# Optimization experiments

Hardware: AMD Instinct MI355X
Metric: run time of the kernel (lower is better)

## Reference

```python
import jax, jax.numpy as jnp
jax.config.update("jax_enable_x64", True)  # morton codes need int64 bit tricks
import numpy as np

B = 8
N_POINTS = 131072
PATCH = 32
STRIDE = 16
RES = 1024
D_MODEL = 256
L = (N_POINTS - PATCH) // STRIDE + 1  # 8191


def setup_inputs() -> dict:
    key = jax.random.key(0)
    ks = jax.random.split(key, 11)
    def lin_w(k, fin, fout):
        return (jax.random.normal(k, (fin, fout), jnp.float32) / np.sqrt(fin)).astype(jnp.float32)
    return {
        "points": jax.random.normal(ks[0], (B, N_POINTS, 3), jnp.float32),
        # LocalGeometryEncoder mlp: 3 -> 64 -> 128 (ReLU after both)
        "W1": lin_w(ks[1], 3, 64), "b1": jnp.zeros((64,), jnp.float32),
        "W2": lin_w(ks[2], 64, 128), "b2": jnp.zeros((128,), jnp.float32),
        # PositionalEncoding mlp: 3 -> 64 -> 128 (ReLU only after first)
        "Wp1": lin_w(ks[3], 3, 64), "bp1": jnp.zeros((64,), jnp.float32),
        "Wp2": lin_w(ks[4], 64, 128), "bp2": jnp.zeros((128,), jnp.float32),
        # projection: 256 -> d_model
        "Wproj": lin_w(ks[5], 256, D_MODEL), "bproj": jnp.zeros((D_MODEL,), jnp.float32),
    }


def _expand_bits(v):
    v = v.astype(jnp.int64)
    v = (v | (v << 32)) & jnp.int64(8725724278095871)
    v = (v | (v << 16)) & jnp.int64(8725728556220671)
    v = (v | (v << 8)) & jnp.int64(1157144660301377551)
    v = (v | (v << 4)) & jnp.int64(1207822528635744451)
    v = (v | (v << 2)) & jnp.int64(1317624576693539401)
    return v


def _morton_code(points):
    p_min = points.min(axis=1, keepdims=True)
    p_max = points.max(axis=1, keepdims=True)
    scale = jnp.clip(p_max - p_min, 1e-8, None)
    normed = (points - p_min) / scale
    q = jnp.clip((normed * (RES - 1)).astype(jnp.int64), 0, RES - 1)  # [B,N,3]
    return _expand_bits(q[..., 0]) * 4 + _expand_bits(q[..., 1]) * 2 + _expand_bits(q[..., 2])


def reference(points, W1, b1, W2, b2, Wp1, bp1, Wp2, bp2, Wproj, bproj):
    # z-order sort
    morton = _morton_code(points)                 # [B,N] int64
    sort_idx = jnp.argsort(morton, axis=1)        # [B,N]
    sp = jnp.take_along_axis(points, sort_idx[..., None], axis=1)  # [B,N,3]
    # sliding-window unfold -> [B,L,P,3]
    win = jnp.arange(L)[:, None] * STRIDE + jnp.arange(PATCH)[None, :]  # [L,P]
    patches = sp[:, win, :]
    # local geometry encoder
    centroids = patches.mean(axis=2)              # [B,L,3]
    local = patches - centroids[:, :, None, :]    # [B,L,P,3]
    h = jax.nn.relu(jnp.einsum('blpc,cd->blpd', local, W1) + b1)
    feat = jax.nn.relu(jnp.einsum('blpd,de->blpe', h, W2) + b2)  # [B,L,P,128]
    geo = feat.max(axis=2)                        # [B,L,128]
    # positional encoding of centroids
    pos = jax.nn.relu(centroids @ Wp1 + bp1) @ Wp2 + bp2  # [B,L,128]
    combined = jnp.concatenate([geo, pos], axis=-1)       # [B,L,256]
    tokens = combined @ Wproj + bproj                     # [B,L,d_model]
    return tokens, centroids, sort_idx
```

## Files before the change

kernel.cpp:

```cpp
#include <hip/hip_runtime.h>
#include <hip/hip_bf16.h>
#include <stdint.h>

#define B_SZ   8
#define N_PTS  131072
#define L_TOK  8191
#define M_TOK  (B_SZ * L_TOK)

typedef unsigned long long u64;
typedef unsigned int u32;
typedef unsigned short u16;
typedef __hip_bfloat16 bf16;
typedef float f32x4 __attribute__((ext_vector_type(4)));
typedef short bf16x8 __attribute__((ext_vector_type(8)));
typedef u32 u32x4 __attribute__((ext_vector_type(4)));

__device__ __forceinline__ u16 f2bf(float f) {
  u32 u = __float_as_uint(f);
  u32 r = u + 0x7FFFu + ((u >> 16) & 1u);
  return (u16)(r >> 16);
}
__device__ __forceinline__ float bf2f(u16 s) {
  return __uint_as_float(((u32)s) << 16);
}

__device__ __forceinline__ void split_pair(float h0, float h1, u32& hp, u32& lp) {
  asm("v_cvt_pk_bf16_f32 %0, %1, %2" : "=v"(hp) : "v"(h0), "v"(h1));
  float r0 = __uint_as_float(hp << 16);
  float r1 = __uint_as_float(hp & 0xFFFF0000u);
  asm("v_cvt_pk_bf16_f32 %0, %1, %2" : "=v"(lp) : "v"(h0 - r0), "v"(h1 - r1));
}
__device__ __forceinline__ bf16x8 asbf(u32x4 x) {
  union { u32x4 a; bf16x8 b; } u; u.a = x; return u.b;
}

__device__ __forceinline__ u32 f2u_mono(float f) {
  u32 u = __float_as_uint(f);
  return (u & 0x80000000u) ? ~u : (u | 0x80000000u);
}
__device__ __forceinline__ float u2f_mono(u32 u) {
  u32 b = (u & 0x80000000u) ? (u ^ 0x80000000u) : ~u;
  return __uint_as_float(b);
}

__global__ void init_mm_kernel(u32* mm) {
  int t = threadIdx.x;
  if (t < 48) mm[t] = ((t % 6) < 3) ? 0xFFFFFFFFu : 0u;
}

__global__ __launch_bounds__(256) void minmax_kernel(const float* __restrict__ pts,
                                                     u32* __restrict__ mm) {
  int b = blockIdx.x >> 6;
  int chunk = blockIdx.x & 63;
  int base = b * N_PTS + chunk * 2048;
  float mn0 = 3.4e38f, mn1 = 3.4e38f, mn2 = 3.4e38f;
  float mx0 = -3.4e38f, mx1 = -3.4e38f, mx2 = -3.4e38f;
  for (int i = threadIdx.x; i < 2048; i += 256) {
    const float* p = pts + (size_t)(base + i) * 3;
    float x = p[0], y = p[1], z = p[2];
    mn0 = fminf(mn0, x); mx0 = fmaxf(mx0, x);
    mn1 = fminf(mn1, y); mx1 = fmaxf(mx1, y);
    mn2 = fminf(mn2, z); mx2 = fmaxf(mx2, z);
  }
  __shared__ u32 smn[3], smx[3];
  if (threadIdx.x < 3) { smn[threadIdx.x] = 0xFFFFFFFFu; smx[threadIdx.x] = 0u; }
  __syncthreads();
  atomicMin(&smn[0], f2u_mono(mn0)); atomicMin(&smn[1], f2u_mono(mn1)); atomicMin(&smn[2], f2u_mono(mn2));
  atomicMax(&smx[0], f2u_mono(mx0)); atomicMax(&smx[1], f2u_mono(mx1)); atomicMax(&smx[2], f2u_mono(mx2));
  __syncthreads();
  if (threadIdx.x < 3)       atomicMin(&mm[b * 6 + threadIdx.x], smn[threadIdx.x]);
  else if (threadIdx.x < 6)  atomicMax(&mm[b * 6 + threadIdx.x], smx[threadIdx.x - 3]);
}

__device__ __forceinline__ u64 expand_bits(u64 v) {
  v = (v | (v << 32)) & 0x001F00000000FFFFull;
  v = (v | (v << 16)) & 0x001F0000FF0000FFull;
  v = (v | (v << 8))  & 0x100F00F00F00F00Full;
  v = (v | (v << 4))  & 0x10C30C30C30C30C3ull;
  v = (v | (v << 2))  & 0x1249249249249249ull;
  return v;
}

__device__ __forceinline__ long long quant1(float p, float mn, float mx) {
  float scale = fmaxf(mx - mn, 1e-8f);
  float num = p - mn;
  float rcp = 1.0f / scale;
  asm volatile("" : "+v"(rcp));
  float normed = num * rcp;
  asm volatile("" : "+v"(normed));
  float scaled = normed * 1023.0f;
  asm volatile("" : "+v"(scaled));
  long long q = (long long)scaled;
  q = q < 0 ? 0 : q; q = q > 1023 ? 1023 : q;
  return q;
}

__global__ __launch_bounds__(256) void morton_kernel(const float* __restrict__ pts,
                                                     const u32* __restrict__ mm,
                                                     u64* __restrict__ keys) {
  int gid = blockIdx.x * 256 + threadIdx.x;
  int b = gid >> 17;
  int i = gid & (N_PTS - 1);
  const u32* mb = mm + b * 6;
  float mn0 = u2f_mono(mb[0]), mn1 = u2f_mono(mb[1]), mn2 = u2f_mono(mb[2]);
  float mx0 = u2f_mono(mb[3]), mx1 = u2f_mono(mb[4]), mx2 = u2f_mono(mb[5]);
  const float* p = pts + (size_t)gid * 3;
  long long q0 = quant1(p[0], mn0, mx0);
  long long q1 = quant1(p[1], mn1, mx1);
  long long q2 = quant1(p[2], mn2, mx2);
  u64 m = expand_bits((u64)q0) * 4ull + expand_bits((u64)q1) * 2ull + expand_bits((u64)q2);
  keys[gid] = (m << 17) | (u64)i;
}

__global__ __launch_bounds__(512) void radix_hist(const u64* __restrict__ keys,
                                                  u32* __restrict__ hist, int shift) {
  int blk = blockIdx.x;
  int b = blk >> 6, c = blk & 63;
  int t = threadIdx.x;
  __shared__ u32 h[256];
  if (t < 256) h[t] = 0;
  __syncthreads();
  size_t base = ((size_t)b << 17) + (size_t)c * 2048;
  #pragma unroll
  for (int i = 0; i < 4; ++i) {
    u32 d = (u32)((keys[base + i * 512 + t] >> shift) & 255u);
    atomicAdd(&h[d], 1u);
  }
  __syncthreads();
  if (t < 256) hist[(blk << 8) + t] = h[t];
}

__global__ __launch_bounds__(256) void radix_scan_a(u32* __restrict__ hist,
                                                    u32* __restrict__ tot) {
  int blk = blockIdx.x;
  int b = blk >> 3, dg = blk & 7;
  int t = threadIdx.x;
  __shared__ u32 H[32 * 65];
  __shared__ u32 part[32 * 8];
  for (int i = t; i < 2048; i += 256) {
    int c = i >> 5, d5 = i & 31;
    H[d5 * 65 + c] = hist[((b * 64 + c) << 8) + dg * 32 + d5];
  }
  __syncthreads();
  int d5 = t & 31, sub = t >> 5;
  u32 s = 0;
  for (int c = sub * 8; c < sub * 8 + 8; ++c) s += H[d5 * 65 + c];
  part[d5 * 8 + sub] = s;
  __syncthreads();
  u32 run = 0;
  for (int k = 0; k < sub; ++k) run += part[d5 * 8 + k];
  if (sub == 7) tot[(b << 8) + dg * 32 + d5] = run + s;
  for (int c = sub * 8; c < sub * 8 + 8; ++c) {
    u32 x = H[d5 * 65 + c];
    H[d5 * 65 + c] = run;
    run += x;
  }
  __syncthreads();
  for (int i = t; i < 2048; i += 256) {
    int c = i >> 5, d5b = i & 31;
    hist[((b * 64 + c) << 8) + dg * 32 + d5b] = H[d5b * 65 + c];
  }
}

__global__ __launch_bounds__(256) void radix_scan_b(const u32* __restrict__ tot,
                                                    u32* __restrict__ dbase) {
  int b = blockIdx.x;
  int t = threadIdx.x;
  __shared__ u32 s[256];
  u32 my = tot[(b << 8) + t];
  s[t] = my;
  __syncthreads();
  for (int off = 1; off < 256; off <<= 1) {
    u32 v = (t >= off) ? s[t - off] : 0u;
    __syncthreads();
    s[t] += v;
    __syncthreads();
  }
  dbase[(b << 8) + t] = s[t] - my;
}

__global__ __launch_bounds__(512) void radix_scatter(const u64* __restrict__ keys_in,
                                                     u64* __restrict__ keys_out,
                                                     const u32* __restrict__ hist,
                                                     const u32* __restrict__ dbase,
                                                     int shift) {
  int blk = blockIdx.x;
  int b = blk >> 6, c = blk & 63;
  int t = threadIdx.x;
  int w = t >> 6, lane = t & 63;
  __shared__ u32 whist[8][256];
  __shared__ u32 gbase[256];
  for (int i = t; i < 2048; i += 512) ((u32*)whist)[i] = 0u;
  if (t < 256) gbase[t] = hist[(blk << 8) + t] + dbase[(b << 8) + t];
  __syncthreads();
  size_t base = ((size_t)b << 17) + (size_t)c * 2048;
  u64 key[4]; u32 dig[4]; u32 loff[4];
  #pragma unroll
  for (int i = 0; i < 4; ++i) {
    key[i] = keys_in[base + w * 256 + i * 64 + lane];
    dig[i] = (u32)((key[i] >> shift) & 255u);
  }
  #pragma unroll
  for (int i = 0; i < 4; ++i) {
    u64 m = ~0ull;
    #pragma unroll
    for (int k = 0; k < 8; ++k) {
      u64 bb = __ballot((dig[i] >> k) & 1u);
      m &= ((dig[i] >> k) & 1u) ? bb : ~bb;
    }
    u32 rank = (u32)__popcll(m & ((1ull << lane) - 1ull));
    u32 cnt = (u32)__popcll(m);
    int leader = (int)__ffsll((unsigned long long)m) - 1;
    u32 prev = 0;
    if (lane == leader) prev = atomicAdd(&whist[w][dig[i]], cnt);
    prev = __shfl(prev, leader);
    loff[i] = prev + rank;
  }
  __syncthreads();
  if (t < 256) {
    u32 run = 0;
    #pragma unroll
    for (int ww = 0; ww < 8; ++ww) { u32 v = whist[ww][t]; whist[ww][t] = run; run += v; }
  }
  __syncthreads();
  #pragma unroll
  for (int i = 0; i < 4; ++i) {
    u32 dst = gbase[dig[i]] + whist[w][dig[i]] + loff[i];
    keys_out[((size_t)b << 17) + dst] = key[i];
  }
}

__global__ __launch_bounds__(256) void extract_frag_kernel(
    const u64* __restrict__ keys, const float* __restrict__ pts,
    float* __restrict__ sp, float* __restrict__ sidx,
    const float* __restrict__ Wproj, const float* __restrict__ W2,
    const float* __restrict__ Wp2,
    u16* __restrict__ wfrag, u16* __restrict__ w2f, u16* __restrict__ wp2f) {
  int bid = blockIdx.x;
  int t = threadIdx.x;
  if (bid < 4096) {
    int gid = bid * 256 + t;
    u64 key = keys[gid];
    int idx = (int)(key & 0x1FFFFull);
    sidx[gid] = (float)idx;
    int b = gid >> 17;
    const float* src = pts + ((size_t)(b << 17) + idx) * 3;
    float* dst = sp + (size_t)gid * 3;
    dst[0] = src[0]; dst[1] = src[1]; dst[2] = src[2];
  } else {
    int fb = bid - 4096;
    if (fb < 256) {
      int e = fb * 256 + t;
      int k = e >> 8, n = e & 255;
      float v = Wproj[e];
      u16 hb = f2bf(v);
      u16 lb = f2bf(v - bf2f(hb));
      int ks = k >> 5, q = (k >> 3) & 3, j = k & 7;
      int nt = n >> 4, ln2 = n & 15;
      int base = ((ks * 16 + nt) * 64 + q * 16 + ln2) * 8 + j;
      wfrag[base] = hb;
      wfrag[65536 + base] = lb;
    } else {
      const float* W = (fb < 288) ? W2 : Wp2;
      u16* frag = (fb < 288) ? w2f : wp2f;
      int e = ((fb < 288) ? (fb - 256) : (fb - 288)) * 256 + t;
      int k = e >> 7, n = e & 127;
      float v = W[e];
      u16 hb = f2bf(v);
      u16 lb = f2bf(v - bf2f(hb));
      int kc = k >> 5, q = (k >> 3) & 3, j = k & 7;
      int nt = n >> 4, ln2 = n & 15;
      int base = ((kc * 8 + nt) * 64 + q * 16 + ln2) * 8 + j;
      frag[base] = hb;
      frag[8192 + base] = lb;
    }
  }
}

__global__ __launch_bounds__(512) void patch_kernel(
    const float* __restrict__ sp,
    const float* __restrict__ W1, const float* __restrict__ b1,
    const u16* __restrict__ W2g, const float* __restrict__ b2,
    const float* __restrict__ Wp1, const float* __restrict__ bp1,
    const u16* __restrict__ Wp2g, const float* __restrict__ bp2,
    bf16* __restrict__ comb, float* __restrict__ cent_out) {
  __shared__ float ptsS[6192];
  __shared__ float cenS[384];
  __shared__ float w1p[256];
  __shared__ float wpp[256];
  __shared__ float b2s[128];
  __shared__ float bp2s[128];
  __shared__ __align__(16) u16 W2frag[16384];

  int t = threadIdx.x;
  int bib = blockIdx.x;
  int b = blockIdx.y;
  int l0 = bib * 128;
  int pcount = min(128, L_TOK - l0);

  {
    const float4* src4 = (const float4*)(sp + (size_t)b * (N_PTS * 3) + (size_t)l0 * 48);
    int nvec = min(1548, ((N_PTS - l0 * 16) * 3) >> 2);
    float4* dst4 = (float4*)ptsS;
    for (int i = t; i < nvec; i += 512) dst4[i] = src4[i];
  }
  {
    const float4* s4 = (const float4*)W2g;
    float4* d4 = (float4*)W2frag;
    for (int i = t; i < 2048; i += 512) d4[i] = s4[i];
  }
  if (t < 64) {
    w1p[t] = W1[t]; w1p[64 + t] = W1[64 + t];
    w1p[128 + t] = W1[128 + t]; w1p[192 + t] = b1[t];
  } else if (t < 128) {
    int i = t - 64;
    wpp[i] = Wp1[i]; wpp[64 + i] = Wp1[64 + i];
    wpp[128 + i] = Wp1[128 + i]; wpp[192 + i] = bp1[i];
  } else if (t < 256) {
    b2s[t - 128] = b2[t - 128];
  } else if (t < 384) {
    bp2s[t - 256] = bp2[t - 256];
  }
  __syncthreads();

  if (t < 384) {
    int pa = t / 3, c = t - pa * 3;
    if (pa < pcount) {
      float s = 0.f;
      for (int i = 0; i < 32; ++i) {
        int ii = (i + pa) & 31;
        s += ptsS[(pa * 16 + ii) * 3 + c];
      }
      float cv = s * (1.0f / 32.0f);
      cenS[pa * 3 + c] = cv;
      cent_out[(size_t)(b * L_TOK + l0 + pa) * 3 + c] = cv;
    }
  }
  __syncthreads();

  int w = t >> 6, lane = t & 63, ln = lane & 15, quad = lane >> 4;
  const bf16x8* Bf = (const bf16x8*)W2frag;

  for (int ig = 0; ig < 16; ++ig) {
    int ll = w * 16 + ig;
    if (ll >= pcount) break;
    float cx = cenS[ll * 3], cy = cenS[ll * 3 + 1], cz = cenS[ll * 3 + 2];
    float xs[2], ys[2], zs[2];
    #pragma unroll
    for (int mt = 0; mt < 2; ++mt) {
      int row = ll * 16 + mt * 16 + ln;
      xs[mt] = ptsS[row * 3] - cx;
      ys[mt] = ptsS[row * 3 + 1] - cy;
      zs[mt] = ptsS[row * 3 + 2] - cz;
    }
    u32x4 Ahi[2][2], Alo[2][2];
    #pragma unroll
    for (int kc = 0; kc < 2; ++kc)
      #pragma unroll
      for (int w4 = 0; w4 < 4; ++w4) {
        int col = kc * 32 + quad * 8 + w4 * 2;
        float wx0 = w1p[col],     wy0 = w1p[64 + col],     wz0 = w1p[128 + col],     wb0 = w1p[192 + col];
        float wx1 = w1p[col + 1], wy1 = w1p[64 + col + 1], wz1 = w1p[128 + col + 1], wb1 = w1p[192 + col + 1];
        #pragma unroll
        for (int mt = 0; mt < 2; ++mt) {
          float h0 = fmaxf(fmaf(xs[mt], wx0, fmaf(ys[mt], wy0, fmaf(zs[mt], wz0, wb0))), 0.f);
          float h1 = fmaxf(fmaf(xs[mt], wx1, fmaf(ys[mt], wy1, fmaf(zs[mt], wz1, wb1))), 0.f);
          u32 hp, lp;
          split_pair(h0, h1, hp, lp);
          Ahi[mt][kc][w4] = hp;
          Alo[mt][kc][w4] = lp;
        }
      }
    bf16x8 Ah[2][2], Al[2][2];
    #pragma unroll
    for (int mt = 0; mt < 2; ++mt)
      #pragma unroll
      for (int kc = 0; kc < 2; ++kc) { Ah[mt][kc] = asbf(Ahi[mt][kc]); Al[mt][kc] = asbf(Alo[mt][kc]); }

    size_t tokoff = (size_t)(b * L_TOK + l0 + ll) * 256;
    #pragma unroll
    for (int half = 0; half < 2; ++half) {
      f32x4 acc[2][4];
      #pragma unroll
      for (int mt = 0; mt < 2; ++mt)
        #pragma unroll
        for (int n4 = 0; n4 < 4; ++n4) acc[mt][n4] = (f32x4){0.f, 0.f, 0.f, 0.f};
      #pragma unroll
      for (int n4 = 0; n4 < 4; ++n4) {
        int nt = half * 4 + n4;
        bf16x8 Bh0 = Bf[(0 * 8 + nt) * 64 + lane];
        bf16x8 Bh1 = Bf[(1 * 8 + nt) * 64 + lane];
        bf16x8 Bl0 = Bf[1024 + (0 * 8 + nt) * 64 + lane];
        bf16x8 Bl1 = Bf[1024 + (1 * 8 + nt) * 64 + lane];
        #pragma unroll
        for (int mt = 0; mt < 2; ++mt) {
          acc[mt][n4] = __builtin_amdgcn_mfma_f32_16x16x32_bf16(Ah[mt][0], Bh0, acc[mt][n4], 0, 0, 0);
          acc[mt][n4] = __builtin_amdgcn_mfma_f32_16x16x32_bf16(Ah[mt][1], Bh1, acc[mt][n4], 0, 0, 0);
          acc[mt][n4] = __builtin_amdgcn_mfma_f32_16x16x32_bf16(Al[mt][0], Bh0, acc[mt][n4], 0, 0, 0);
          acc[mt][n4] = __builtin_amdgcn_mfma_f32_16x16x32_bf16(Al[mt][1], Bh1, acc[mt][n4], 0, 0, 0);
          acc[mt][n4] = __builtin_amdgcn_mfma_f32_16x16x32_bf16(Ah[mt][0], Bl0, acc[mt][n4], 0, 0, 0);
          acc[mt][n4] = __builtin_amdgcn_mfma_f32_16x16x32_bf16(Ah[mt][1], Bl1, acc[mt][n4], 0, 0, 0);
        }
      }
      #pragma unroll
      for (int n4 = 0; n4 < 4; ++n4) {
        int col = (half * 4 + n4) * 16 + ln;
        float bv = b2s[col];
        float m = 0.f;
        #pragma unroll
        for (int mt = 0; mt < 2; ++mt)
          #pragma unroll
          for (int r = 0; r < 4; ++r) m = fmaxf(m, acc[mt][n4][r] + bv);
        m = fmaxf(m, __shfl_xor(m, 16));
        m = fmaxf(m, __shfl_xor(m, 32));
        if (lane < 16) comb[tokoff + col] = __float2bfloat16(m);
      }
    }
  }

  {
    int lrow = w * 16 + ln;
    int lcl = min(lrow, pcount - 1);
    float cx = cenS[lcl * 3], cy = cenS[lcl * 3 + 1], cz = cenS[lcl * 3 + 2];
    u32x4 Ahi[2], Alo[2];
    #pragma unroll
    for (int kc = 0; kc < 2; ++kc)
      #pragma unroll
      for (int w4 = 0; w4 < 4; ++w4) {
        int col = kc * 32 + quad * 8 + w4 * 2;
        float h0 = fmaxf(fmaf(cx, wpp[col], fmaf(cy, wpp[64 + col], fmaf(cz, wpp[128 + col], wpp[192 + col]))), 0.f);
        float h1 = fmaxf(fmaf(cx, wpp[col + 1], fmaf(cy, wpp[64 + col + 1], fmaf(cz, wpp[128 + col + 1], wpp[192 + col + 1]))), 0.f);
        u32 hp, lp;
        split_pair(h0, h1, hp, lp);
        Ahi[kc][w4] = hp;
        Alo[kc][w4] = lp;
      }
    bf16x8 A0h = asbf(Ahi[0]), A1h = asbf(Ahi[1]), A0l = asbf(Alo[0]), A1l = asbf(Alo[1]);
    const bf16x8* Pf = (const bf16x8*)Wp2g;
    f32x4 acc[8];
    #pragma unroll
    for (int nt = 0; nt < 8; ++nt) acc[nt] = (f32x4){0.f, 0.f, 0.f, 0.f};
    #pragma unroll
    for (int nt = 0; nt < 8; ++nt) {
      bf16x8 Bh0 = Pf[(0 * 8 + nt) * 64 + lane];
      bf16x8 Bh1 = Pf[(8 + nt) * 64 + lane];
      bf16x8 Bl0 = Pf[1024 + (0 * 8 + nt) * 64 + lane];
      bf16x8 Bl1 = Pf[1024 + (8 + nt) * 64 + lane];
      acc[nt] = __builtin_amdgcn_mfma_f32_16x16x32_bf16(A0h, Bh0, acc[nt], 0, 0, 0);
      acc[nt] = __builtin_amdgcn_mfma_f32_16x16x32_bf16(A1h, Bh1, acc[nt], 0, 0, 0);
      acc[nt] = __builtin_amdgcn_mfma_f32_16x16x32_bf16(A0l, Bh0, acc[nt], 0, 0, 0);
      acc[nt] = __builtin_amdgcn_mfma_f32_16x16x32_bf16(A1l, Bh1, acc[nt], 0, 0, 0);
      acc[nt] = __builtin_amdgcn_mfma_f32_16x16x32_bf16(A0h, Bl0, acc[nt], 0, 0, 0);
      acc[nt] = __builtin_amdgcn_mfma_f32_16x16x32_bf16(A1h, Bl1, acc[nt], 0, 0, 0);
    }
    #pragma unroll
    for (int nt = 0; nt < 8; ++nt)
      #pragma unroll
      for (int r = 0; r < 4; ++r) {
        int lr = w * 16 + quad * 4 + r;
        if (lr < pcount) {
          float v = acc[nt][r] + bp2s[nt * 16 + ln];
          comb[(size_t)(b * L_TOK + l0 + lr) * 256 + 128 + nt * 16 + ln] = __float2bfloat16(v);
        }
      }
  }
}

__global__ __launch_bounds__(256) void proj_mfma(const bf16* __restrict__ A,
                                                 const u16* __restrict__ fragG,
                                                 const float* __restrict__ bias,
                                                 float* __restrict__ C) {
  int t = threadIdx.x;
  int w = t >> 6, lane = t & 63, ln = lane & 15, quad = lane >> 4;
  int mg = blockIdx.x >> 1;
  int nh = blockIdx.x & 1;
  int tile0 = mg * 16 + w * 4;
  const bf16x8* Bf = (const bf16x8*)fragG;

  bf16x8 Af[4][8];
  const bf16x8 zero8 = (bf16x8){0, 0, 0, 0, 0, 0, 0, 0};
  #pragma unroll
  for (int mt = 0; mt < 4; ++mt) {
    int row = (tile0 + mt) * 16 + ln;
    bool ok = row < M_TOK;
    const bf16x8* ap = (const bf16x8*)(A + (size_t)(ok ? row : 0) * 256);
    #pragma unroll
    for (int ks = 0; ks < 8; ++ks) {
      bf16x8 v = ap[ks * 4 + quad];
      Af[mt][ks] = ok ? v : zero8;
    }
  }

  for (int nt2 = 0; nt2 < 8; ++nt2) {
    int nt = nh * 8 + nt2;
    f32x4 acc[4];
    #pragma unroll
    for (int mt = 0; mt < 4; ++mt) acc[mt] = (f32x4){0.f, 0.f, 0.f, 0.f};
    #pragma unroll
    for (int ks = 0; ks < 8; ++ks) {
      bf16x8 Bh = Bf[(ks * 16 + nt) * 64 + lane];
      bf16x8 Bl = Bf[8192 + (ks * 16 + nt) * 64 + lane];
      #pragma unroll
      for (int mt = 0; mt < 4; ++mt)
        acc[mt] = __builtin_amdgcn_mfma_f32_16x16x32_bf16(Af[mt][ks], Bh, acc[mt], 0, 0, 0);
      #pragma unroll
      for (int mt = 0; mt < 4; ++mt)
        acc[mt] = __builtin_amdgcn_mfma_f32_16x16x32_bf16(Af[mt][ks], Bl, acc[mt], 0, 0, 0);
    }
    int col = nt * 16 + ln;
    float bv = bias[col];
    #pragma unroll
    for (int mt = 0; mt < 4; ++mt)
      #pragma unroll
      for (int r = 0; r < 4; ++r) {
        int row = (tile0 + mt) * 16 + quad * 4 + r;
        if (row < M_TOK) C[(size_t)row * 256 + col] = acc[mt][r] + bv;
      }
  }
}

extern "C" void kernel_launch(void* const* d_in, const int* in_sizes, int n_in,
                              void* d_out, int out_size, void* d_ws, size_t ws_size,
                              hipStream_t stream) {
  const float* points = (const float*)d_in[0];
  const float* W1 = (const float*)d_in[1];
  const float* b1 = (const float*)d_in[2];
  const float* W2 = (const float*)d_in[3];
  const float* b2 = (const float*)d_in[4];
  const float* Wp1 = (const float*)d_in[5];
  const float* bp1 = (const float*)d_in[6];
  const float* Wp2 = (const float*)d_in[7];
  const float* bp2 = (const float*)d_in[8];
  const float* Wproj = (const float*)d_in[9];
  const float* bproj = (const float*)d_in[10];

  float* out = (float*)d_out;
  float* tokens = out;
  float* cents  = out + 16775168;
  float* sidx   = out + 16971752;

  char* ws = (char*)d_ws;
  u32* mm     = (u32*)ws;
  u64* keysA  = (u64*)(ws + 256);
  float* sp   = (float*)(ws + 256 + 8388608);
  char* combB = ws + 256 + 8388608 + 12582912;
  bf16* comb  = (bf16*)combB;
  u64* keysB  = (u64*)combB;
  u32* hist   = (u32*)(combB + 8388608);
  u32* totG   = (u32*)(combB + 8388608 + 2097152);
  u32* dbase  = (u32*)(combB + 8388608 + 2097152 + 8192);
  u16* wfrag  = (u16*)(ws + 256);
  u16* w2fg   = (u16*)(ws + 256 + 262144);
  u16* wp2fg  = (u16*)(ws + 256 + 262144 + 32768);

  init_mm_kernel<<<1, 64, 0, stream>>>(mm);
  minmax_kernel<<<512, 256, 0, stream>>>(points, mm);
  morton_kernel<<<4096, 256, 0, stream>>>(points, mm, keysA);

  const int shifts[4] = {17, 25, 33, 41};
  u64* src = keysA; u64* dst = keysB;
  for (int p = 0; p < 4; ++p) {
    radix_hist<<<512, 512, 0, stream>>>(src, hist, shifts[p]);
    radix_scan_a<<<64, 256, 0, stream>>>(hist, totG);
    radix_scan_b<<<8, 256, 0, stream>>>(totG, dbase);
    radix_scatter<<<512, 512, 0, stream>>>(src, dst, hist, dbase, shifts[p]);
    u64* tmp = src; src = dst; dst = tmp;
  }

  extract_frag_kernel<<<4416, 256, 0, stream>>>(src, points, sp, sidx,
                                                Wproj, W2, Wp2, wfrag, w2fg, wp2fg);
  patch_kernel<<<dim3(64, 8), 512, 0, stream>>>(sp, W1, b1, w2fg, b2,
                                                Wp1, bp1, wp2fg, bp2, comb, cents);
  proj_mfma<<<512, 256, 0, stream>>>(comb, wfrag, bproj, tokens);
}
```

Before: 352.1 us.

## Fuse radix digit-total scan into scatter and final pass into gather

Digit totals are now accumulated with global atomics in the histogram kernel, and each scatter block redoes the small 256-entry exclusive scan itself, so the separate scan_b kernel goes away. The last radix pass writes the sorted indices and gathered points directly instead of writing keys and running a separate extract kernel. The init kernel becomes memsets. This cuts kernel launches and one full pass over the keys, at the cost of redundant per-block scans and extra global atomics.

```diff
diff --git a/kernel.cpp b/kernel.cpp
--- a/kernel.cpp
+++ b/kernel.cpp
@@ -41,11 +41,6 @@
 __device__ __forceinline__ float u2f_mono(u32 u) {
   u32 b = (u & 0x80000000u) ? (u ^ 0x80000000u) : ~u;
   return __uint_as_float(b);
-}
-
-__global__ void init_mm_kernel(u32* mm) {
-  int t = threadIdx.x;
-  if (t < 48) mm[t] = ((t % 6) < 3) ? 0xFFFFFFFFu : 0u;
 }
 
 __global__ __launch_bounds__(256) void minmax_kernel(const float* __restrict__ pts,
@@ -68,8 +63,8 @@
   atomicMin(&smn[0], f2u_mono(mn0)); atomicMin(&smn[1], f2u_mono(mn1)); atomicMin(&smn[2], f2u_mono(mn2));
   atomicMax(&smx[0], f2u_mono(mx0)); atomicMax(&smx[1], f2u_mono(mx1)); atomicMax(&smx[2], f2u_mono(mx2));
   __syncthreads();
-  if (threadIdx.x < 3)       atomicMin(&mm[b * 6 + threadIdx.x], smn[threadIdx.x]);
-  else if (threadIdx.x < 6)  atomicMax(&mm[b * 6 + threadIdx.x], smx[threadIdx.x - 3]);
+  if (threadIdx.x < 3)       atomicMin(&mm[b * 3 + threadIdx.x], smn[threadIdx.x]);
+  else if (threadIdx.x < 6)  atomicMax(&mm[24 + b * 3 + threadIdx.x - 3], smx[threadIdx.x - 3]);
 }
 
 __device__ __forceinline__ u64 expand_bits(u64 v) {
@@ -101,9 +96,8 @@
   int gid = blockIdx.x * 256 + threadIdx.x;
   int b = gid >> 17;
   int i = gid & (N_PTS - 1);
-  const u32* mb = mm + b * 6;
-  float mn0 = u2f_mono(mb[0]), mn1 = u2f_mono(mb[1]), mn2 = u2f_mono(mb[2]);
-  float mx0 = u2f_mono(mb[3]), mx1 = u2f_mono(mb[4]), mx2 = u2f_mono(mb[5]);
+  float mn0 = u2f_mono(mm[b * 3]), mn1 = u2f_mono(mm[b * 3 + 1]), mn2 = u2f_mono(mm[b * 3 + 2]);
+  float mx0 = u2f_mono(mm[24 + b * 3]), mx1 = u2f_mono(mm[24 + b * 3 + 1]), mx2 = u2f_mono(mm[24 + b * 3 + 2]);
   const float* p = pts + (size_t)gid * 3;
   long long q0 = quant1(p[0], mn0, mx0);
   long long q1 = quant1(p[1], mn1, mx1);
@@ -113,7 +107,8 @@
 }
 
 __global__ __launch_bounds__(512) void radix_hist(const u64* __restrict__ keys,
-                                                  u32* __restrict__ hist, int shift) {
+                                                  u32* __restrict__ hist,
+                                                  u32* __restrict__ tot, int shift) {
   int blk = blockIdx.x;
   int b = blk >> 6, c = blk & 63;
   int t = threadIdx.x;
@@ -127,11 +122,14 @@
     atomicAdd(&h[d], 1u);
   }
   __syncthreads();
-  if (t < 256) hist[(blk << 8) + t] = h[t];
-}
-
-__global__ __launch_bounds__(256) void radix_scan_a(u32* __restrict__ hist,
-                                                    u32* __restrict__ tot) {
+  if (t < 256) {
+    u32 v = h[t];
+    hist[(blk << 8) + t] = v;
+    if (v) atomicAdd(&tot[(b << 8) + t], v);
+  }
+}
+
+__global__ __launch_bounds__(256) void radix_scan_a(u32* __restrict__ hist) {
   int blk = blockIdx.x;
   int b = blk >> 3, dg = blk & 7;
   int t = threadIdx.x;
@@ -149,7 +147,6 @@
   __syncthreads();
   u32 run = 0;
   for (int k = 0; k < sub; ++k) run += part[d5 * 8 + k];
-  if (sub == 7) tot[(b << 8) + dg * 32 + d5] = run + s;
   for (int c = sub * 8; c < sub * 8 + 8; ++c) {
     u32 x = H[d5 * 65 + c];
     H[d5 * 65 + c] = run;
@@ -162,27 +159,10 @@
   }
 }
 
-__global__ __launch_bounds__(256) void radix_scan_b(const u32* __restrict__ tot,
-                                                    u32* __restrict__ dbase) {
-  int b = blockIdx.x;
-  int t = threadIdx.x;
-  __shared__ u32 s[256];
-  u32 my = tot[(b << 8) + t];
-  s[t] = my;
-  __syncthreads();
-  for (int off = 1; off < 256; off <<= 1) {
-    u32 v = (t >= off) ? s[t - off] : 0u;
-    __syncthreads();
-    s[t] += v;
-    __syncthreads();
-  }
-  dbase[(b << 8) + t] = s[t] - my;
-}
-
 __global__ __launch_bounds__(512) void radix_scatter(const u64* __restrict__ keys_in,
                                                      u64* __restrict__ keys_out,
                                                      const u32* __restrict__ hist,
-                                                     const u32* __restrict__ dbase,
+                                                     const u32* __restrict__ tot,
                                                      int shift) {
   int blk = blockIdx.x;
   int b = blk >> 6, c = blk & 63;
@@ -190,9 +170,23 @@
   int w = t >> 6, lane = t & 63;
   __shared__ u32 whist[8][256];
   __shared__ u32 gbase[256];
+  __shared__ u32 sd[256];
   for (int i = t; i < 2048; i += 512) ((u32*)whist)[i] = 0u;
-  if (t < 256) gbase[t] = hist[(blk << 8) + t] + dbase[(b << 8) + t];
-  __syncthreads();
+  u32 my = 0;
+  if (t < 256) {
+    my = tot[(b << 8) + t];
+    sd[t] = my;
+    gbase[t] = hist[(blk << 8) + t];
+  }
+  __syncthreads();
+  #pragma unroll
+  for (int off = 1; off < 256; off <<= 1) {
+    u32 v = (t >= off && t < 256) ? sd[t - off] : 0u;
+    __syncthreads();
+    if (t < 256) sd[t] += v;
+    __syncthreads();
+  }
+  if (t < 256) gbase[t] += sd[t] - my;
   size_t base = ((size_t)b << 17) + (size_t)c * 2048;
   u64 key[4]; u32 dig[4]; u32 loff[4];
   #pragma unroll
@@ -230,27 +224,19 @@
   }
 }
 
-__global__ __launch_bounds__(256) void extract_frag_kernel(
-    const u64* __restrict__ keys, const float* __restrict__ pts,
-    float* __restrict__ sp, float* __restrict__ sidx,
+__global__ __launch_bounds__(512) void scatter_final(
+    const u64* __restrict__ keys_in, const u32* __restrict__ hist,
+    const u32* __restrict__ tot,
+    const float* __restrict__ pts, float* __restrict__ sp, float* __restrict__ sidx,
     const float* __restrict__ Wproj, const float* __restrict__ W2,
     const float* __restrict__ Wp2,
     u16* __restrict__ wfrag, u16* __restrict__ w2f, u16* __restrict__ wp2f) {
   int bid = blockIdx.x;
   int t = threadIdx.x;
-  if (bid < 4096) {
-    int gid = bid * 256 + t;
-    u64 key = keys[gid];
-    int idx = (int)(key & 0x1FFFFull);
-    sidx[gid] = (float)idx;
-    int b = gid >> 17;
-    const float* src = pts + ((size_t)(b << 17) + idx) * 3;
-    float* dst = sp + (size_t)gid * 3;
-    dst[0] = src[0]; dst[1] = src[1]; dst[2] = src[2];
-  } else {
-    int fb = bid - 4096;
-    if (fb < 256) {
-      int e = fb * 256 + t;
+  if (bid >= 512) {
+    int fb = bid - 512;
+    if (fb < 128) {
+      int e = fb * 512 + t;
       int k = e >> 8, n = e & 255;
       float v = Wproj[e];
       u16 hb = f2bf(v);
@@ -261,9 +247,9 @@
       wfrag[base] = hb;
       wfrag[65536 + base] = lb;
     } else {
-      const float* W = (fb < 288) ? W2 : Wp2;
-      u16* frag = (fb < 288) ? w2f : wp2f;
-      int e = ((fb < 288) ? (fb - 256) : (fb - 288)) * 256 + t;
+      const float* W = (fb < 144) ? W2 : Wp2;
+      u16* frag = (fb < 144) ? w2f : wp2f;
+      int e = ((fb < 144) ? (fb - 128) : (fb - 144)) * 512 + t;
       int k = e >> 7, n = e & 127;
       float v = W[e];
       u16 hb = f2bf(v);
@@ -274,6 +260,69 @@
       frag[base] = hb;
       frag[8192 + base] = lb;
     }
+    return;
+  }
+  int blk = bid;
+  int b = blk >> 6, c = blk & 63;
+  int w = t >> 6, lane = t & 63;
+  __shared__ u32 whist[8][256];
+  __shared__ u32 gbase[256];
+  __shared__ u32 sd[256];
+  for (int i = t; i < 2048; i += 512) ((u32*)whist)[i] = 0u;
+  u32 my = 0;
+  if (t < 256) {
+    my = tot[(b << 8) + t];
+    sd[t] = my;
+    gbase[t] = hist[(blk << 8) + t];
+  }
+  __syncthreads();
+  #pragma unroll
+  for (int off = 1; off < 256; off <<= 1) {
+    u32 v = (t >= off && t < 256) ? sd[t - off] : 0u;
+    __syncthreads();
+    if (t < 256) sd[t] += v;
+    __syncthreads();
+  }
+  if (t < 256) gbase[t] += sd[t] - my;
+  size_t base = ((size_t)b << 17) + (size_t)c * 2048;
+  u64 key[4]; u32 dig[4]; u32 loff[4];
+  #pragma unroll
+  for (int i = 0; i < 4; ++i) {
+    key[i] = keys_in[base + w * 256 + i * 64 + lane];
+    dig[i] = (u32)((key[i] >> 41) & 255u);
+  }
+  #pragma unroll
+  for (int i = 0; i < 4; ++i) {
+    u64 m = ~0ull;
+    #pragma unroll
+    for (int k = 0; k < 8; ++k) {
+      u64 bb = __ballot((dig[i] >> k) & 1u);
+      m &= ((dig[i] >> k) & 1u) ? bb : ~bb;
+    }
+    u32 rank = (u32)__popcll(m & ((1ull << lane) - 1ull));
+    u32 cnt = (u32)__popcll(m);
+    int leader = (int)__ffsll((unsigned long long)m) - 1;
+    u32 prev = 0;
+    if (lane == leader) prev = atomicAdd(&whist[w][dig[i]], cnt);
+    prev = __shfl(prev, leader);
+    loff[i] = prev + rank;
+  }
+  __syncthreads();
+  if (t < 256) {
+    u32 run = 0;
+    #pragma unroll
+    for (int ww = 0; ww < 8; ++ww) { u32 v = whist[ww][t]; whist[ww][t] = run; run += v; }
+  }
+  __syncthreads();
+  #pragma unroll
+  for (int i = 0; i < 4; ++i) {
+    u32 dst = gbase[dig[i]] + whist[w][dig[i]] + loff[i];
+    int idx = (int)(key[i] & 0x1FFFFull);
+    u32 gid = ((u32)b << 17) + dst;
+    sidx[gid] = (float)idx;
+    const float* s = pts + ((size_t)(b << 17) + idx) * 3;
+    float* dp = sp + (size_t)gid * 3;
+    dp[0] = s[0]; dp[1] = s[1]; dp[2] = s[2];
   }
 }
 
@@ -548,27 +597,29 @@
   u64* keysB  = (u64*)combB;
   u32* hist   = (u32*)(combB + 8388608);
   u32* totG   = (u32*)(combB + 8388608 + 2097152);
-  u32* dbase  = (u32*)(combB + 8388608 + 2097152 + 8192);
   u16* wfrag  = (u16*)(ws + 256);
   u16* w2fg   = (u16*)(ws + 256 + 262144);
   u16* wp2fg  = (u16*)(ws + 256 + 262144 + 32768);
 
-  init_mm_kernel<<<1, 64, 0, stream>>>(mm);
+  hipMemsetAsync(mm, 0xFF, 96, stream);
+  hipMemsetAsync((char*)mm + 96, 0x00, 96, stream);
+  hipMemsetAsync(totG, 0x00, 4 * 2048 * 4, stream);
   minmax_kernel<<<512, 256, 0, stream>>>(points, mm);
   morton_kernel<<<4096, 256, 0, stream>>>(points, mm, keysA);
 
   const int shifts[4] = {17, 25, 33, 41};
   u64* src = keysA; u64* dst = keysB;
-  for (int p = 0; p < 4; ++p) {
-    radix_hist<<<512, 512, 0, stream>>>(src, hist, shifts[p]);
-    radix_scan_a<<<64, 256, 0, stream>>>(hist, totG);
-    radix_scan_b<<<8, 256, 0, stream>>>(totG, dbase);
-    radix_scatter<<<512, 512, 0, stream>>>(src, dst, hist, dbase, shifts[p]);
+  for (int p = 0; p < 3; ++p) {
+    radix_hist<<<512, 512, 0, stream>>>(src, hist, totG + p * 2048, shifts[p]);
+    radix_scan_a<<<64, 256, 0, stream>>>(hist);
+    radix_scatter<<<512, 512, 0, stream>>>(src, dst, hist, totG + p * 2048, shifts[p]);
     u64* tmp = src; src = dst; dst = tmp;
   }
-
-  extract_frag_kernel<<<4416, 256, 0, stream>>>(src, points, sp, sidx,
-                                                Wproj, W2, Wp2, wfrag, w2fg, wp2fg);
+  radix_hist<<<512, 512, 0, stream>>>(src, hist, totG + 3 * 2048, shifts[3]);
+  radix_scan_a<<<64, 256, 0, stream>>>(hist);
+  scatter_final<<<672, 512, 0, stream>>>(src, hist, totG + 3 * 2048, points, sp, sidx,
+                                         Wproj, W2, Wp2, wfrag, w2fg, wp2fg);
+
   patch_kernel<<<dim3(64, 8), 512, 0, stream>>>(sp, W1, b1, w2fg, b2,
                                                 Wp1, bp1, wp2fg, bp2, comb, cents);
   proj_mfma<<<512, 256, 0, stream>>>(comb, wfrag, bproj, tokens);
```

After: 349.5 us (median of 2 runs). Within noise of the previous version (-0.7%).
